# Performance work log

Measured on AMD Instinct MI355X. Metric: run time of the kernel, lower is better.

## Reference

```python
import jax, jax.numpy as jnp
import numpy as np

PIXEL_SIZE = 0.1
PI = 3.141592653589793


def setup_inputs() -> dict:
    key = jax.random.key(0)
    batch = jax.random.normal(key, (128, 1, 512, 512), dtype=jnp.float32)
    return {"batch": batch}


def _hann_window(roi):
    # lin = linspace(-roi/2, roi/2, roi); r[i,j] = sqrt(lin[j]^2 + lin[i]^2)
    lin = jnp.linspace(-roi / 2, roi / 2, roi, dtype=jnp.float32)
    r = jnp.sqrt(lin[None, :] ** 2 + lin[:, None] ** 2)
    hann = 0.5 * (1.0 + jnp.cos(PI * r / (roi / 2)))
    hann = jnp.where(r > roi / 2, 0.0, hann)
    return hann  # [roi, roi]


def _radial_segments(roi, n_freq):
    # radialDst = round(sqrt(xx^2 + yy^2)) with x = arange(-cx, roi-cx)
    cx = roi // 2
    x = np.arange(-cx, roi - cx, dtype=np.float64)
    xx, yy = np.meshgrid(x, x, indexing="ij")
    rad = np.round(np.sqrt(xx ** 2 + yy ** 2)).astype(np.int32)
    # bins >= n_freq go into an overflow segment that is discarded
    seg = np.where(rad < n_freq, rad, n_freq)
    return jnp.asarray(seg.ravel())


def reference(batch):
    px = PIXEL_SIZE
    roi = batch.shape[-1]
    cx = roi // 2
    n_freq = cx + 1
    nyquist = 1.0 / (2.0 * px)

    # subtract per-ROI mean
    batch_nm = batch - jnp.mean(batch, axis=(2, 3), keepdims=True)

    # Hann-windowed 2D power spectrum, averaged over realizations
    hann = _hann_window(roi)[None, None, :, :]
    F = jnp.fft.fftshift(jnp.fft.fft2(batch_nm * hann, axes=(2, 3)), axes=(2, 3))
    ps = jnp.mean(jnp.abs(F) ** 2, axis=0)            # [1, roi, roi]
    nps2D = (px ** 2 / roi ** 2) * jnp.squeeze(ps)    # [roi, roi]

    # single-pass radial mean binning (replaces per-k boolean-mask loop)
    seg = _radial_segments(roi, n_freq)
    flat = nps2D.ravel()
    sums = jax.ops.segment_sum(flat, seg, num_segments=n_freq + 1)[:n_freq]
    counts = jax.ops.segment_sum(jnp.ones_like(flat), seg, num_segments=n_freq + 1)[:n_freq]
    nps1D = sums / counts

    f1D = jnp.linspace(0.0, nyquist, n_freq, dtype=jnp.float32)
    return nps1D, nps2D, f1D
```

## Files before the change

### kernel.cpp

```cpp
#include <hip/hip_runtime.h>

#define N 512
#define NF 257
#define NB 128
#define PI_F 3.14159265358979323846f
#define C_SQ2 0.70710678118654752440f

__device__ __forceinline__ float2 cmul(float2 a, float2 b) {
    return make_float2(a.x * b.x - a.y * b.y, a.x * b.y + a.y * b.x);
}
__device__ __forceinline__ void bf(float2& a, float2& b) {
    float2 t = b;
    b = make_float2(a.x - t.x, a.y - t.y);
    a = make_float2(a.x + t.x, a.y + t.y);
}
__device__ __forceinline__ void bf_tw(float2& a, float2& b, float2 w) {
    float2 t = cmul(b, w);
    b = make_float2(a.x - t.x, a.y - t.y);
    a = make_float2(a.x + t.x, a.y + t.y);
}
__device__ __forceinline__ void bf_ni(float2& a, float2& b) {
    float2 t = make_float2(b.y, -b.x);
    b = make_float2(a.x - t.x, a.y - t.y);
    a = make_float2(a.x + t.x, a.y + t.y);
}
__device__ __forceinline__ void lds_fence() {
    asm volatile("s_waitcnt lgkmcnt(0)" ::: "memory");
}

__device__ __forceinline__ void fft512(float2 v[8], float* lre, float* lim, int l) {
    const float2 w64  = make_float2(C_SQ2, -C_SQ2);
    const float2 w192 = make_float2(-C_SQ2, -C_SQ2);
    bf(v[0], v[1]); bf(v[2], v[3]); bf(v[4], v[5]); bf(v[6], v[7]);
    bf(v[0], v[2]); bf_ni(v[1], v[3]); bf(v[4], v[6]); bf_ni(v[5], v[7]);
    bf(v[0], v[4]); bf_tw(v[1], v[5], w64); bf_ni(v[2], v[6]); bf_tw(v[3], v[7], w192);
#pragma unroll
    for (int e = 0; e < 8; e++) { lre[9 * l + e] = v[e].x; lim[9 * l + e] = v[e].y; }
    lds_fence();
    int g = l >> 3, r = l & 7;
#pragma unroll
    for (int t = 0; t < 8; t++) {
        int p = 72 * g + 9 * t + r;
        v[t].x = lre[p]; v[t].y = lim[p];
    }
    float sn, cs;
    sincosf(-(PI_F / 32.0f) * (float)r, &sn, &cs);
    float2 W1 = make_float2(cs, sn);
    float2 W2 = cmul(W1, W1);
    float2 W3 = cmul(W2, W2);
    float2 W2n = make_float2(W2.y, -W2.x);
    bf_tw(v[0], v[1], W3); bf_tw(v[2], v[3], W3); bf_tw(v[4], v[5], W3); bf_tw(v[6], v[7], W3);
    bf_tw(v[0], v[2], W2); bf_tw(v[1], v[3], W2n); bf_tw(v[4], v[6], W2); bf_tw(v[5], v[7], W2n);
    {
        float2 W1a = cmul(W1, w64);
        float2 W1n = make_float2(W1.y, -W1.x);
        float2 W1c = cmul(W1, w192);
        bf_tw(v[0], v[4], W1); bf_tw(v[1], v[5], W1a); bf_tw(v[2], v[6], W1n); bf_tw(v[3], v[7], W1c);
    }
#pragma unroll
    for (int t = 0; t < 8; t++) {
        int p = 72 * g + 9 * t + r;
        lre[p] = v[t].x; lim[p] = v[t].y;
    }
    lds_fence();
#pragma unroll
    for (int t = 0; t < 8; t++) {
        int p = 72 * t + l + (l >> 3);
        v[t].x = lre[p]; v[t].y = lim[p];
    }
    sincosf(-(PI_F / 256.0f) * (float)l, &sn, &cs);
    float2 Wc = make_float2(cs, sn);
    float2 w2 = cmul(Wc, Wc);
    float2 w4 = cmul(w2, w2);
    float2 w2n = make_float2(w2.y, -w2.x);
    bf_tw(v[0], v[1], w4); bf_tw(v[2], v[3], w4); bf_tw(v[4], v[5], w4); bf_tw(v[6], v[7], w4);
    bf_tw(v[0], v[2], w2); bf_tw(v[1], v[3], w2n); bf_tw(v[4], v[6], w2); bf_tw(v[5], v[7], w2n);
    {
        float2 Wca = cmul(Wc, w64);
        float2 Wcn = make_float2(Wc.y, -Wc.x);
        float2 Wcc = cmul(Wc, w192);
        bf_tw(v[0], v[4], Wc); bf_tw(v[1], v[5], Wca); bf_tw(v[2], v[6], Wcn); bf_tw(v[3], v[7], Wcc);
    }
}

__global__ void zero_kernel(float* __restrict__ acc, float* __restrict__ bins,
                            float* __restrict__ meanacc) {
    int i = blockIdx.x * blockDim.x + threadIdx.x;
    if (i < N * N) acc[i] = 0.0f;
    if (i < 2 * (NF + 1)) bins[i] = 0.0f;
    if (i < NB) meanacc[i] = 0.0f;
}

__global__ __launch_bounds__(256) void meanpart_kernel(const float* __restrict__ x,
                                                       float* __restrict__ meanacc) {
    int b = blockIdx.y;
    const float4* p = (const float4*)(x + (size_t)b * N * N) + blockIdx.x * 4096;
    float s = 0.0f;
#pragma unroll
    for (int it = 0; it < 16; it++) {
        float4 v = p[it * 256 + threadIdx.x];
        s += (v.x + v.y) + (v.z + v.w);
    }
#pragma unroll
    for (int off = 32; off > 0; off >>= 1) s += __shfl_down(s, off);
    __shared__ float red[4];
    if ((threadIdx.x & 63) == 0) red[threadIdx.x >> 6] = s;
    __syncthreads();
    if (threadIdx.x == 0)
        atomicAdd(meanacc + b, (red[0] + red[1]) + (red[2] + red[3]));
}

__global__ __launch_bounds__(512) void rowfft_kernel(const float* __restrict__ x,
                                                     const float* __restrict__ meanacc,
                                                     float2* __restrict__ inter) {
    __shared__ float sm[9216];
    int tid = threadIdx.x;
    int w = tid >> 6, l = tid & 63;
    int img = blockIdx.x >> 5;
    int rowbase = (blockIdx.x & 31) << 4;
    int r1 = rowbase + 2 * w, r2 = r1 + 1;
    float mn = meanacc[img] * (1.0f / ((float)N * (float)N));
    const float* x1 = x + ((size_t)img * N + r1) * N;
    const float* x2 = x1 + N;

    const float step = (float)N / (float)(N - 1);
    float a1 = -0.5f * (float)N + (float)r1 * step;
    float a2 = -0.5f * (float)N + (float)r2 * step;
    float a1s = a1 * a1, a2s = a2 * a2;

    float2 v[8];
    int rl = __brev((unsigned)l) >> 26;
#pragma unroll
    for (int e = 0; e < 8; e++) {
        int src = (int)((__brev((unsigned)e) >> 29) << 6) + rl;
        float lc = -0.5f * (float)N + (float)src * step;
        float lc2 = lc * lc;
        float rr1 = sqrtf(a1s + lc2), rr2 = sqrtf(a2s + lc2);
        float h1 = (rr1 > 256.0f) ? 0.0f : 0.5f * (1.0f + cosf(PI_F * rr1 * (1.0f / 256.0f)));
        float h2 = (rr2 > 256.0f) ? 0.0f : 0.5f * (1.0f + cosf(PI_F * rr2 * (1.0f / 256.0f)));
        v[e].x = (x1[src] - mn) * h1;
        v[e].y = (x2[src] - mn) * h2;
    }

    float* lre = sm + w * 1152;
    float* lim = lre + 576;
    fft512(v, lre, lim, l);
    __syncthreads();

    float* tre = sm;
    float* tim = sm + 4240;
    int lr0 = 2 * w, lr1 = lr0 + 1;
    int sl = (64 - l) & 63;
#pragma unroll
    for (int t = 0; t <= 4; t++) {
        float2 a = v[7 - t];
        float zfx = __shfl(a.x, sl);
        float zfy = __shfl(a.y, sl);
        if (l == 0) { float2 o = v[(8 - t) & 7]; zfx = o.x; zfy = o.y; }
        float2 z = v[t];
        int col = 64 * t + l;
        if (col < NF) {
            tre[lr0 * 265 + col] = 0.5f * (z.x + zfx);
            tim[lr0 * 265 + col] = 0.5f * (z.y - zfy);
            tre[lr1 * 265 + col] = 0.5f * (z.y + zfy);
            tim[lr1 * 265 + col] = 0.5f * (zfx - z.x);
        }
    }
    __syncthreads();

    int c0 = tid >> 4, rr = tid & 15;
#pragma unroll
    for (int it = 0; it < 9; it++) {
        int c = it * 32 + c0;
        if (c < NF) {
            float2 val = make_float2(tre[rr * 265 + c], tim[rr * 265 + c]);
            inter[((size_t)img * NF + c) * N + rowbase + rr] = val;
        }
    }
}

__global__ __launch_bounds__(512) void colfft_kernel(const float2* __restrict__ inter,
                                                     float* __restrict__ accT) {
    __shared__ float sm[9216];
    int tid = threadIdx.x;
    int w = tid >> 6, l = tid & 63;
    int col = blockIdx.x * 8 + w;
    int colc = col < NF ? col : NF - 1;
    int b0 = blockIdx.y * 8;
    float* lre = sm + w * 1152;
    float* lim = lre + 576;
    int rl = __brev((unsigned)l) >> 26;

    float pw[8];
#pragma unroll
    for (int t = 0; t < 8; t++) pw[t] = 0.0f;

    for (int bi = 0; bi < 8; bi++) {
        const float2* base = inter + ((size_t)(b0 + bi) * NF + colc) * N;
        float2 v[8];
#pragma unroll
        for (int e = 0; e < 8; e++)
            v[e] = base[(int)((__brev((unsigned)e) >> 29) << 6) + rl];
        fft512(v, lre, lim, l);
#pragma unroll
        for (int t = 0; t < 8; t++)
            pw[t] += v[t].x * v[t].x + v[t].y * v[t].y;
    }

    if (col < NF) {
        int sv = (col + 256) & 511;
#pragma unroll
        for (int t = 0; t < 8; t++) {
            int k = 64 * t + l;
            int su = (k + 256) & 511;
            atomicAdd(&accT[(size_t)sv * N + su], pw[t]);
        }
        if (col >= 1 && col <= 255) {
            int sv2 = (768 - col) & 511;
#pragma unroll
            for (int t = 0; t < 8; t++) {
                int k = 64 * t + l;
                int su2 = (768 - k) & 511;
                atomicAdd(&accT[(size_t)sv2 * N + su2], pw[t]);
            }
        }
    }
}

__global__ __launch_bounds__(256) void finalize2d_kernel(const float* __restrict__ accT,
                                                         float* __restrict__ out2d,
                                                         float* __restrict__ bins) {
    __shared__ float lsum[NF];
    __shared__ float lcnt[NF];
    int t = threadIdx.x;
    for (int i = t; i < NF; i += 256) { lsum[i] = 0.0f; lcnt[i] = 0.0f; }
    __syncthreads();
    const float scale = (0.1f * 0.1f) / ((float)N * (float)N) / (float)NB;
    int idx = blockIdx.x * 256 + t;
    int stride = gridDim.x * 256;
    for (int p = idx; p < N * N; p += stride) {
        int i = p >> 9, j = p & (N - 1);
        float v = accT[(size_t)j * N + i] * scale;
        out2d[p] = v;
        float xi = (float)(i - N / 2), yj = (float)(j - N / 2);
        int rad = (int)rintf(sqrtf(xi * xi + yj * yj));
        if (rad < NF) {
            atomicAdd(&lsum[rad], v);
            atomicAdd(&lcnt[rad], 1.0f);
        }
    }
    __syncthreads();
    for (int i = t; i < NF; i += 256) {
        if (lsum[i] != 0.0f || lcnt[i] != 0.0f) {
            atomicAdd(&bins[i], lsum[i]);
            atomicAdd(&bins[NF + 1 + i], lcnt[i]);
        }
    }
}

__global__ void finalize1d_kernel(const float* __restrict__ bins, float* __restrict__ out) {
    int t = blockIdx.x * blockDim.x + threadIdx.x;
    if (t < NF) {
        out[t] = bins[t] / bins[NF + 1 + t];
        out[NF + N * N + t] = (float)t * (5.0f / 256.0f);
    }
}

extern "C" void kernel_launch(void* const* d_in, const int* in_sizes, int n_in,
                              void* d_out, int out_size, void* d_ws, size_t ws_size,
                              hipStream_t stream) {
    const float* x = (const float*)d_in[0];
    float* out = (float*)d_out;
    char* ws = (char*)d_ws;

    float* accT    = (float*)ws;
    float* meanacc = (float*)(ws + (size_t)N * N * sizeof(float));
    float* bins    = meanacc + NB;
    size_t off_inter = (size_t)N * N * sizeof(float) + NB * sizeof(float)
                       + 2 * (NF + 1) * sizeof(float);
    off_inter = (off_inter + 255) & ~(size_t)255;
    float2* inter = (float2*)(ws + off_inter);

    zero_kernel<<<dim3((N * N + 255) / 256), dim3(256), 0, stream>>>(accT, bins, meanacc);
    meanpart_kernel<<<dim3(16, NB), dim3(256), 0, stream>>>(x, meanacc);
    rowfft_kernel<<<dim3(NB * 32), dim3(512), 0, stream>>>(x, meanacc, inter);
    colfft_kernel<<<dim3(33, 16), dim3(512), 0, stream>>>(inter, accT);
    finalize2d_kernel<<<dim3(256), dim3(256), 0, stream>>>(accT, out + NF, bins);
    finalize1d_kernel<<<dim3(2), dim3(256), 0, stream>>>(bins, out);
}
```

Baseline: 308.0 us.

## Fold mean subtraction into column FFT via linearity, removing separate mean pass

Because the FFT is linear, FFT((x-m)·h) = FFT(x·h) - m·FFT(h). The row FFT therefore runs on the raw windowed input and accumulates each image's sum in the same pass. A small new kernel computes the row-FFT of the Hann window once, and the column FFT subtracts mean times that window spectrum before transforming. This drops the separate mean kernel's extra read of the whole input. The change also uses fast sincos/cos intrinsics, prefetches the next image's column data in the column FFT with smaller blocks, and makes finalize read accT coalesced while writing transposed. The risks are lower intrinsic precision and an added dependency on cross-block atomics finishing before the column pass.

```diff
diff --git a/kernel.cpp b/kernel.cpp
--- a/kernel.cpp
+++ b/kernel.cpp
@@ -44,7 +44,7 @@
         v[t].x = lre[p]; v[t].y = lim[p];
     }
     float sn, cs;
-    sincosf(-(PI_F / 32.0f) * (float)r, &sn, &cs);
+    __sincosf(-(PI_F / 32.0f) * (float)r, &sn, &cs);
     float2 W1 = make_float2(cs, sn);
     float2 W2 = cmul(W1, W1);
     float2 W3 = cmul(W2, W2);
@@ -68,7 +68,7 @@
         int p = 72 * t + l + (l >> 3);
         v[t].x = lre[p]; v[t].y = lim[p];
     }
-    sincosf(-(PI_F / 256.0f) * (float)l, &sn, &cs);
+    __sincosf(-(PI_F / 256.0f) * (float)l, &sn, &cs);
     float2 Wc = make_float2(cs, sn);
     float2 w2 = cmul(Wc, Wc);
     float2 w4 = cmul(w2, w2);
@@ -91,37 +91,12 @@
     if (i < NB) meanacc[i] = 0.0f;
 }
 
-__global__ __launch_bounds__(256) void meanpart_kernel(const float* __restrict__ x,
-                                                       float* __restrict__ meanacc) {
-    int b = blockIdx.y;
-    const float4* p = (const float4*)(x + (size_t)b * N * N) + blockIdx.x * 4096;
-    float s = 0.0f;
-#pragma unroll
-    for (int it = 0; it < 16; it++) {
-        float4 v = p[it * 256 + threadIdx.x];
-        s += (v.x + v.y) + (v.z + v.w);
-    }
-#pragma unroll
-    for (int off = 32; off > 0; off >>= 1) s += __shfl_down(s, off);
-    __shared__ float red[4];
-    if ((threadIdx.x & 63) == 0) red[threadIdx.x >> 6] = s;
-    __syncthreads();
-    if (threadIdx.x == 0)
-        atomicAdd(meanacc + b, (red[0] + red[1]) + (red[2] + red[3]));
-}
-
-__global__ __launch_bounds__(512) void rowfft_kernel(const float* __restrict__ x,
-                                                     const float* __restrict__ meanacc,
-                                                     float2* __restrict__ inter) {
+__global__ __launch_bounds__(512) void hannfft_kernel(float2* __restrict__ Hrow) {
     __shared__ float sm[9216];
     int tid = threadIdx.x;
     int w = tid >> 6, l = tid & 63;
-    int img = blockIdx.x >> 5;
-    int rowbase = (blockIdx.x & 31) << 4;
+    int rowbase = blockIdx.x << 4;
     int r1 = rowbase + 2 * w, r2 = r1 + 1;
-    float mn = meanacc[img] * (1.0f / ((float)N * (float)N));
-    const float* x1 = x + ((size_t)img * N + r1) * N;
-    const float* x2 = x1 + N;
 
     const float step = (float)N / (float)(N - 1);
     float a1 = -0.5f * (float)N + (float)r1 * step;
@@ -138,8 +113,8 @@
         float rr1 = sqrtf(a1s + lc2), rr2 = sqrtf(a2s + lc2);
         float h1 = (rr1 > 256.0f) ? 0.0f : 0.5f * (1.0f + cosf(PI_F * rr1 * (1.0f / 256.0f)));
         float h2 = (rr2 > 256.0f) ? 0.0f : 0.5f * (1.0f + cosf(PI_F * rr2 * (1.0f / 256.0f)));
-        v[e].x = (x1[src] - mn) * h1;
-        v[e].y = (x2[src] - mn) * h2;
+        v[e].x = h1;
+        v[e].y = h2;
     }
 
     float* lre = sm + w * 1152;
@@ -174,33 +149,136 @@
         int c = it * 32 + c0;
         if (c < NF) {
             float2 val = make_float2(tre[rr * 265 + c], tim[rr * 265 + c]);
-            inter[((size_t)img * NF + c) * N + rowbase + rr] = val;
-        }
-    }
-}
-
-__global__ __launch_bounds__(512) void colfft_kernel(const float2* __restrict__ inter,
-                                                     float* __restrict__ accT) {
+            Hrow[(size_t)c * N + rowbase + rr] = val;
+        }
+    }
+}
+
+__global__ __launch_bounds__(512) void rowfft_kernel(const float* __restrict__ x,
+                                                     float* __restrict__ meanacc,
+                                                     float2* __restrict__ inter) {
     __shared__ float sm[9216];
+    __shared__ float redsum[8];
     int tid = threadIdx.x;
     int w = tid >> 6, l = tid & 63;
-    int col = blockIdx.x * 8 + w;
+    int img = blockIdx.x >> 5;
+    int rowbase = (blockIdx.x & 31) << 4;
+    int r1 = rowbase + 2 * w, r2 = r1 + 1;
+    const float* x1 = x + ((size_t)img * N + r1) * N;
+    const float* x2 = x1 + N;
+
+    const float step = (float)N / (float)(N - 1);
+    float a1 = -0.5f * (float)N + (float)r1 * step;
+    float a2 = -0.5f * (float)N + (float)r2 * step;
+    float a1s = a1 * a1, a2s = a2 * a2;
+
+    float2 v[8];
+    float rsum = 0.0f;
+    int rl = __brev((unsigned)l) >> 26;
+#pragma unroll
+    for (int e = 0; e < 8; e++) {
+        int src = (int)((__brev((unsigned)e) >> 29) << 6) + rl;
+        float lc = -0.5f * (float)N + (float)src * step;
+        float lc2 = lc * lc;
+        float rr1 = sqrtf(a1s + lc2), rr2 = sqrtf(a2s + lc2);
+        float h1 = (rr1 > 256.0f) ? 0.0f : 0.5f * (1.0f + __cosf(rr1 * (PI_F / 256.0f)));
+        float h2 = (rr2 > 256.0f) ? 0.0f : 0.5f * (1.0f + __cosf(rr2 * (PI_F / 256.0f)));
+        float xv1 = x1[src], xv2 = x2[src];
+        rsum += xv1 + xv2;
+        v[e].x = xv1 * h1;
+        v[e].y = xv2 * h2;
+    }
+#pragma unroll
+    for (int off = 32; off > 0; off >>= 1) rsum += __shfl_down(rsum, off);
+    if (l == 0) redsum[w] = rsum;
+
+    float* lre = sm + w * 1152;
+    float* lim = lre + 576;
+    fft512(v, lre, lim, l);
+    __syncthreads();
+    if (tid == 0) {
+        float s = 0.0f;
+#pragma unroll
+        for (int i = 0; i < 8; i++) s += redsum[i];
+        atomicAdd(meanacc + img, s);
+    }
+
+    float* tre = sm;
+    float* tim = sm + 4240;
+    int lr0 = 2 * w, lr1 = lr0 + 1;
+    int sl = (64 - l) & 63;
+#pragma unroll
+    for (int t = 0; t <= 4; t++) {
+        float2 a = v[7 - t];
+        float zfx = __shfl(a.x, sl);
+        float zfy = __shfl(a.y, sl);
+        if (l == 0) { float2 o = v[(8 - t) & 7]; zfx = o.x; zfy = o.y; }
+        float2 z = v[t];
+        int col = 64 * t + l;
+        if (col < NF) {
+            tre[lr0 * 265 + col] = 0.5f * (z.x + zfx);
+            tim[lr0 * 265 + col] = 0.5f * (z.y - zfy);
+            tre[lr1 * 265 + col] = 0.5f * (z.y + zfy);
+            tim[lr1 * 265 + col] = 0.5f * (zfx - z.x);
+        }
+    }
+    __syncthreads();
+
+    int c0 = tid >> 4, rr = tid & 15;
+#pragma unroll
+    for (int it = 0; it < 9; it++) {
+        int c = it * 32 + c0;
+        if (c < NF) {
+            float2 val = make_float2(tre[rr * 265 + c], tim[rr * 265 + c]);
+            inter[((size_t)img * NF + c) * N + rowbase + rr] = val;
+        }
+    }
+}
+
+__global__ __launch_bounds__(256) void colfft_kernel(const float2* __restrict__ inter,
+                                                     const float2* __restrict__ Hrow,
+                                                     const float* __restrict__ meanacc,
+                                                     float* __restrict__ accT) {
+    __shared__ float sm[4608];
+    int tid = threadIdx.x;
+    int w = tid >> 6, l = tid & 63;
+    int col = blockIdx.x * 4 + w;
     int colc = col < NF ? col : NF - 1;
     int b0 = blockIdx.y * 8;
     float* lre = sm + w * 1152;
     float* lim = lre + 576;
     int rl = __brev((unsigned)l) >> 26;
 
+    int off[8];
+#pragma unroll
+    for (int e = 0; e < 8; e++)
+        off[e] = (int)((__brev((unsigned)e) >> 29) << 6) + rl;
+
+    float2 hv[8];
+    const float2* hbase = Hrow + (size_t)colc * N;
+#pragma unroll
+    for (int e = 0; e < 8; e++) hv[e] = hbase[off[e]];
+
     float pw[8];
 #pragma unroll
     for (int t = 0; t < 8; t++) pw[t] = 0.0f;
 
+    float2 nv[8];
+    const float2* base0 = inter + ((size_t)b0 * NF + colc) * N;
+#pragma unroll
+    for (int e = 0; e < 8; e++) nv[e] = base0[off[e]];
+
     for (int bi = 0; bi < 8; bi++) {
-        const float2* base = inter + ((size_t)(b0 + bi) * NF + colc) * N;
+        float mn = meanacc[b0 + bi] * (1.0f / ((float)N * (float)N));
         float2 v[8];
 #pragma unroll
         for (int e = 0; e < 8; e++)
-            v[e] = base[(int)((__brev((unsigned)e) >> 29) << 6) + rl];
+            v[e] = make_float2(nv[e].x - mn * hv[e].x, nv[e].y - mn * hv[e].y);
+        if (bi < 7) {
+            const float2* nb = inter + ((size_t)(b0 + bi + 1) * NF + colc) * N;
+#pragma unroll
+            for (int e = 0; e < 8; e++) nv[e] = nb[off[e]];
+        }
         fft512(v, lre, lim, l);
 #pragma unroll
         for (int t = 0; t < 8; t++)
@@ -238,10 +316,10 @@
     const float scale = (0.1f * 0.1f) / ((float)N * (float)N) / (float)NB;
     int idx = blockIdx.x * 256 + t;
     int stride = gridDim.x * 256;
-    for (int p = idx; p < N * N; p += stride) {
-        int i = p >> 9, j = p & (N - 1);
-        float v = accT[(size_t)j * N + i] * scale;
-        out2d[p] = v;
+    for (int q = idx; q < N * N; q += stride) {
+        int j = q >> 9, i = q & (N - 1);
+        float v = accT[q] * scale;
+        out2d[(size_t)i * N + j] = v;
         float xi = (float)(i - N / 2), yj = (float)(j - N / 2);
         int rad = (int)rintf(sqrtf(xi * xi + yj * yj));
         if (rad < NF) {
@@ -276,15 +354,18 @@
     float* accT    = (float*)ws;
     float* meanacc = (float*)(ws + (size_t)N * N * sizeof(float));
     float* bins    = meanacc + NB;
-    size_t off_inter = (size_t)N * N * sizeof(float) + NB * sizeof(float)
-                       + 2 * (NF + 1) * sizeof(float);
+    size_t off_h = (size_t)N * N * sizeof(float) + NB * sizeof(float)
+                   + 2 * (NF + 1) * sizeof(float);
+    off_h = (off_h + 255) & ~(size_t)255;
+    float2* Hrow = (float2*)(ws + off_h);
+    size_t off_inter = off_h + (size_t)NF * N * sizeof(float2);
     off_inter = (off_inter + 255) & ~(size_t)255;
     float2* inter = (float2*)(ws + off_inter);
 
     zero_kernel<<<dim3((N * N + 255) / 256), dim3(256), 0, stream>>>(accT, bins, meanacc);
-    meanpart_kernel<<<dim3(16, NB), dim3(256), 0, stream>>>(x, meanacc);
+    hannfft_kernel<<<dim3(32), dim3(512), 0, stream>>>(Hrow);
     rowfft_kernel<<<dim3(NB * 32), dim3(512), 0, stream>>>(x, meanacc, inter);
-    colfft_kernel<<<dim3(33, 16), dim3(512), 0, stream>>>(inter, accT);
+    colfft_kernel<<<dim3(65, 16), dim3(256), 0, stream>>>(inter, Hrow, meanacc, accT);
     finalize2d_kernel<<<dim3(256), dim3(256), 0, stream>>>(accT, out + NF, bins);
     finalize1d_kernel<<<dim3(2), dim3(256), 0, stream>>>(bins, out);
 }
```

Result: faster. 276.5 us (-10.2%).
